# Performance work log

Measured on AMD Instinct MI355X. Metric: run time of the kernel, lower is better.

Reference implementation:

```python
import jax, jax.numpy as jnp
import numpy as np

B, S, D, H = 4, 2048, 1024, 16
DK = D // H

def setup_inputs() -> dict:
    key = jax.random.key(0)
    ks = jax.random.split(key, 5)
    std = np.sqrt(2.0 / (D + D)).astype(np.float32)
    return {
        "x": jax.random.normal(ks[0], (B, S, D), dtype=jnp.float32),
        "W_q": jax.random.normal(ks[1], (D, D), dtype=jnp.float32) * std,
        "W_k": jax.random.normal(ks[2], (D, D), dtype=jnp.float32) * std,
        "W_v": jax.random.normal(ks[3], (D, D), dtype=jnp.float32) * std,
        "W_o": jax.random.normal(ks[4], (D, D), dtype=jnp.float32) * std,
    }

def reference(x, W_q, W_k, W_v, W_o):
    b, s, d = x.shape
    # Linear layers: y = x @ W.T  (W stored as [out, in])
    q = (x @ W_q.T).reshape(b, s, H, DK).transpose(0, 2, 1, 3)  # [b,h,s,dk]
    k = (x @ W_k.T).reshape(b, s, H, DK).transpose(0, 2, 1, 3)
    v = (x @ W_v.T).reshape(b, s, H, DK).transpose(0, 2, 1, 3)
    scale = 1.0 / jnp.sqrt(jnp.asarray(DK, dtype=x.dtype))
    scores = jnp.einsum("bhqd,bhkd->bhqk", q, k) * scale  # [b,h,s,s]
    causal = jnp.tril(jnp.ones((s, s), dtype=bool))
    scores = jnp.where(causal, scores, jnp.asarray(-jnp.inf, dtype=scores.dtype))
    attn = jax.nn.softmax(scores, axis=-1)
    out = jnp.einsum("bhqk,bhkd->bhqd", attn, v)  # [b,h,s,dk]
    out = out.transpose(0, 2, 1, 3).reshape(b, s, d)
    return out @ W_o.T
```

## Files before the change

### kernel.cpp

```cpp
#include <hip/hip_runtime.h>
#include <stdint.h>

#define B_  4
#define S_  2048
#define D_  1024
#define H_  16
#define DK_ 64
#define M_  (B_ * S_)

typedef __attribute__((ext_vector_type(4))) float  f32x4;
typedef __attribute__((ext_vector_type(8))) __bf16 bf16x8;
typedef __attribute__((ext_vector_type(4))) unsigned short us4;

__device__ __forceinline__ unsigned short cvt_bf16(float f) {
  unsigned u = __float_as_uint(f);
  return (unsigned short)((u + 0x7fffu + ((u >> 16) & 1u)) >> 16);
}

__device__ __forceinline__ f32x4 mfma16(bf16x8 a, bf16x8 b, f32x4 c) {
  return __builtin_amdgcn_mfma_f32_16x16x32_bf16(a, b, c, 0, 0, 0);
}

__device__ __forceinline__ void async16(const void* g, void* l) {
  __builtin_amdgcn_global_load_lds(
      (const __attribute__((address_space(1))) void*)g,
      (__attribute__((address_space(3))) void*)l, 16, 0, 0);
}

#define XN4_ 2097152
#define WN4_ 262144
__global__ void cast_all(const float* __restrict__ x,
                         const float* __restrict__ wq,
                         const float* __restrict__ wk,
                         const float* __restrict__ wv,
                         const float* __restrict__ wo,
                         unsigned short* __restrict__ dst) {
  const int i = blockIdx.x * blockDim.x + threadIdx.x;
  const float* src;
  int k;
  if (i < XN4_) {
    src = x; k = i;
  } else {
    const int j = i - XN4_;
    const int wsel = j >> 18;
    k = j & (WN4_ - 1);
    src = (wsel == 0) ? wq : (wsel == 1) ? wk : (wsel == 2) ? wv : wo;
  }
  f32x4 v = ((const f32x4*)src)[k];
  us4 o;
  o[0] = cvt_bf16(v[0]); o[1] = cvt_bf16(v[1]);
  o[2] = cvt_bf16(v[2]); o[3] = cvt_bf16(v[3]);
  ((us4*)dst)[i] = o;
}

template <int OUTMODE>
__global__ __launch_bounds__(256) void gemm_bt(
    const unsigned short* __restrict__ A,
    const unsigned short* __restrict__ Bm,
    void* __restrict__ Cp,
    unsigned short* __restrict__ Qo, unsigned short* __restrict__ Ko,
    unsigned short* __restrict__ Vto,
    int Ndim, int Kdim) {
  constexpr int BM = 128, BN = 128, BK = 32;
  __shared__ __align__(16) unsigned short As[BM * BK];
  __shared__ __align__(16) unsigned short Bs[BN * BK];

  const int tid = threadIdx.x;
  const int w = tid >> 6, l = tid & 63;
  const int l16 = l & 15, lg = l >> 4;
  const int wr = w >> 1, wc = w & 1;
  const int rowA0 = blockIdx.y * BM;
  const int rowB0 = blockIdx.x * BN;
  const int l4 = l >> 2;
  const int lk = (l & 3) * 8;

  f32x4 acc[4][4] = {};

  for (int kt = 0; kt < Kdim; kt += BK) {
#pragma unroll
    for (int j = 0; j < 2; ++j) {
      const int chunk = j * 4 + w;
      const int r = chunk * 16 + l4;
      async16(A  + (size_t)(rowA0 + r) * Kdim + kt + lk, &As[chunk * 512]);
      async16(Bm + (size_t)(rowB0 + r) * Kdim + kt + lk, &Bs[chunk * 512]);
    }
    __syncthreads();
    bf16x8 af[4], bfr[4];
#pragma unroll
    for (int m = 0; m < 4; ++m)
      af[m] = *(const bf16x8*)&As[(wr * 64 + m * 16 + l16) * BK + lg * 8];
#pragma unroll
    for (int n = 0; n < 4; ++n)
      bfr[n] = *(const bf16x8*)&Bs[(wc * 64 + n * 16 + l16) * BK + lg * 8];
#pragma unroll
    for (int m = 0; m < 4; ++m)
#pragma unroll
      for (int n = 0; n < 4; ++n)
        acc[m][n] = mfma16(af[m], bfr[n], acc[m][n]);
    __syncthreads();
  }

  const int rb = rowA0 + wr * 64;
  const int cb = rowB0 + wc * 64;
  if constexpr (OUTMODE == 2) {
    float* C = (float*)Cp;
#pragma unroll
    for (int m = 0; m < 4; ++m)
#pragma unroll
      for (int n = 0; n < 4; ++n) {
        const int r0 = rb + m * 16 + lg * 4;
        const int c0 = cb + n * 16 + l16;
#pragma unroll
        for (int j = 0; j < 4; ++j)
          C[(size_t)(r0 + j) * Ndim + c0] = acc[m][n][j];
      }
  } else {
    const int region = cb >> 10;
    const int cbl = cb & 1023;
    if (region < 2) {
      unsigned short* C = region ? Ko : Qo;
#pragma unroll
      for (int m = 0; m < 4; ++m)
#pragma unroll
        for (int n = 0; n < 4; ++n) {
          const int r0 = rb + m * 16 + lg * 4;
          const int c0 = cbl + n * 16 + l16;
#pragma unroll
          for (int j = 0; j < 4; ++j)
            C[(size_t)(r0 + j) * 1024 + c0] = cvt_bf16(acc[m][n][j]);
        }
    } else {
#pragma unroll
      for (int m = 0; m < 4; ++m)
#pragma unroll
        for (int n = 0; n < 4; ++n) {
          const int r0 = rb + m * 16 + lg * 4;
          const int c0 = cbl + n * 16 + l16;
          us4 v;
#pragma unroll
          for (int j = 0; j < 4; ++j) v[j] = cvt_bf16(acc[m][n][j]);
          *(us4*)&Vto[((size_t)(r0 >> 11) * 1024 + c0) * 2048 + (r0 & 2047)] = v;
        }
    }
  }
}


#define KS_ 0.1803368801f

#define SMX(sc, mr, sr, oa, P, diag, rb, kv0)                                \
  do {                                                                       \
    if (diag) {                                                              \
      _Pragma("unroll") for (int nc_ = 0; nc_ < 4; ++nc_) {                  \
        const int col_ = (kv0) + nc_ * 16 + l16;                             \
        _Pragma("unroll") for (int j_ = 0; j_ < 4; ++j_)                     \
            if (col_ > (rb) + j_) sc[nc_][j_] = -INFINITY;                   \
      }                                                                      \
    }                                                                        \
    _Pragma("unroll") for (int j_ = 0; j_ < 4; ++j_) {                       \
      float t_ = fmaxf(fmaxf(sc[0][j_], sc[1][j_]),                          \
                       fmaxf(sc[2][j_], sc[3][j_]));                         \
      t_ = fmaxf(t_, __shfl_xor(t_, 1));                                     \
      t_ = fmaxf(t_, __shfl_xor(t_, 2));                                     \
      t_ = fmaxf(t_, __shfl_xor(t_, 4));                                     \
      t_ = fmaxf(t_, __shfl_xor(t_, 8));                                     \
      const bool st_ = __all(t_ <= mr[j_]);     \
      const float mnew_ = st_ ? mr[j_] : fmaxf(mr[j_], t_);                  \
      float rs_ = 0.f;                                                       \
      _Pragma("unroll") for (int nc_ = 0; nc_ < 4; ++nc_) {                  \
        const float p_ = exp2f((sc[nc_][j_] - mnew_) * KS_);                 \
        rs_ += p_;                                                           \
        P[lg * 4 + j_][nc_ * 16 + l16] = cvt_bf16(p_);                       \
      }                                                                      \
      rs_ += __shfl_xor(rs_, 1);                                             \
      rs_ += __shfl_xor(rs_, 2);                                             \
      rs_ += __shfl_xor(rs_, 4);                                             \
      rs_ += __shfl_xor(rs_, 8);                                             \
      if (st_) {                                                             \
        sr[j_] += rs_;                                                       \
      } else {                                                               \
        const float al_ = exp2f((mr[j_] - mnew_) * KS_);                     \
        sr[j_] = sr[j_] * al_ + rs_;                                         \
        mr[j_] = mnew_;                                                      \
        _Pragma("unroll") for (int d_ = 0; d_ < 4; ++d_) oa[d_][j_] *= al_;  \
      }                                                                      \
    }                                                                        \
  } while (0)

__global__ __launch_bounds__(256, 4) void flash_attn(
    const unsigned short* __restrict__ Q,
    const unsigned short* __restrict__ K,
    const unsigned short* __restrict__ Vt,
    unsigned short* __restrict__ O) {
  const int bid  = blockIdx.x;
  const int virt = (bid & 7) * 128 + (bid >> 3);
  const int bh   = virt >> 4;
  const int x    = virt & 15;
  const int b = bh >> 4, h = bh & 15;
  const int tid = threadIdx.x;
  const int w = tid >> 6, l = tid & 63;
  const int l16 = l & 15, lg = l >> 4;

  __shared__ __align__(16) unsigned short Ks[64 * 64];
  __shared__ __align__(16) unsigned short Vs[64 * 64];
  __shared__ __align__(16) unsigned short PA[4][16][72];
  __shared__ __align__(16) unsigned short PB[4][16][72];

  const int tA = x, tB = 31 - x;

  const size_t qkbase = (size_t)(b * S_) * D_ + h * DK_;
  const size_t vbase  = ((size_t)(b * D_) + h * DK_) * S_;

  const int rA = tA * 64 + w * 16 + l16;
  const int rB = tB * 64 + w * 16 + l16;
  bf16x8 qfA[2], qfB[2];
  qfA[0] = *(const bf16x8*)&Q[qkbase + (size_t)rA * D_ + lg * 8];
  qfA[1] = *(const bf16x8*)&Q[qkbase + (size_t)rA * D_ + 32 + lg * 8];
  qfB[0] = *(const bf16x8*)&Q[qkbase + (size_t)rB * D_ + lg * 8];
  qfB[1] = *(const bf16x8*)&Q[qkbase + (size_t)rB * D_ + 32 + lg * 8];

  float mA[4], sA[4], mB[4], sB[4];
  f32x4 oA[4] = {}, oB[4] = {};
#pragma unroll
  for (int j = 0; j < 4; ++j) {
    mA[j] = mB[j] = -INFINITY;
    sA[j] = sB[j] = 0.f;
  }

  const int rbA = tA * 64 + w * 16 + lg * 4;
  const int rbB = tB * 64 + w * 16 + lg * 4;

  for (int kv = 0; kv <= tB; ++kv) {
    const int kv0 = kv * 64;
    if (kv) __syncthreads();
#pragma unroll
    for (int c = 0; c < 2; ++c) {
      const int ci = c * 256 + w * 64;
      const int i  = ci + l;
      const int r  = i >> 3;
      const int cc = (i & 7) ^ (r & 7);
      async16(K  + qkbase + (size_t)(kv0 + r) * D_ + cc * 8, &Ks[ci * 8]);
      async16(Vt + vbase  + (size_t)r * S_ + kv0 + cc * 8,   &Vs[ci * 8]);
    }
    __syncthreads();

    if (kv <= tA) {
      f32x4 sc[4] = {};
      __builtin_amdgcn_s_setprio(1);
#pragma unroll
      for (int nc = 0; nc < 4; ++nc) {
        const int r = nc * 16 + l16;
#pragma unroll
        for (int ks = 0; ks < 2; ++ks) {
          const int byte = (r * 128 + ks * 64 + lg * 16) ^ ((r & 7) << 4);
          bf16x8 kf = *(const bf16x8*)((const char*)Ks + byte);
          sc[nc] = mfma16(qfA[ks], kf, sc[nc]);
        }
      }
      __builtin_amdgcn_s_setprio(0);
      SMX(sc, mA, sA, oA, PA[w], kv == tA, rbA, kv0);
      __asm__ volatile("s_waitcnt lgkmcnt(0)" ::: "memory");
      bf16x8 pa0 = *(const bf16x8*)&PA[w][l16][lg * 8];
      bf16x8 pa1 = *(const bf16x8*)&PA[w][l16][32 + lg * 8];
      __builtin_amdgcn_s_setprio(1);
#pragma unroll
      for (int d = 0; d < 4; ++d) {
        const int r = d * 16 + l16;
#pragma unroll
        for (int ks = 0; ks < 2; ++ks) {
          const int byte = (r * 128 + ks * 64 + lg * 16) ^ ((r & 7) << 4);
          bf16x8 vf = *(const bf16x8*)((const char*)Vs + byte);
          oA[d] = mfma16(ks ? pa1 : pa0, vf, oA[d]);
        }
      }
      __builtin_amdgcn_s_setprio(0);
    }

    {
      f32x4 sc[4] = {};
      __builtin_amdgcn_s_setprio(1);
#pragma unroll
      for (int nc = 0; nc < 4; ++nc) {
        const int r = nc * 16 + l16;
#pragma unroll
        for (int ks = 0; ks < 2; ++ks) {
          const int byte = (r * 128 + ks * 64 + lg * 16) ^ ((r & 7) << 4);
          bf16x8 kf = *(const bf16x8*)((const char*)Ks + byte);
          sc[nc] = mfma16(qfB[ks], kf, sc[nc]);
        }
      }
      __builtin_amdgcn_s_setprio(0);
      SMX(sc, mB, sB, oB, PB[w], kv == tB, rbB, kv0);
      __asm__ volatile("s_waitcnt lgkmcnt(0)" ::: "memory");
      bf16x8 pb0 = *(const bf16x8*)&PB[w][l16][lg * 8];
      bf16x8 pb1 = *(const bf16x8*)&PB[w][l16][32 + lg * 8];
      __builtin_amdgcn_s_setprio(1);
#pragma unroll
      for (int d = 0; d < 4; ++d) {
        const int r = d * 16 + l16;
#pragma unroll
        for (int ks = 0; ks < 2; ++ks) {
          const int byte = (r * 128 + ks * 64 + lg * 16) ^ ((r & 7) << 4);
          bf16x8 vf = *(const bf16x8*)((const char*)Vs + byte);
          oB[d] = mfma16(ks ? pb1 : pb0, vf, oB[d]);
        }
      }
      __builtin_amdgcn_s_setprio(0);
    }
  }

#pragma unroll
  for (int j = 0; j < 4; ++j) {
    const float iA = __builtin_amdgcn_rcpf(sA[j]);
    const float iB = __builtin_amdgcn_rcpf(sB[j]);
#pragma unroll
    for (int d = 0; d < 4; ++d) {
      O[((size_t)(b * S_) + rbA + j) * D_ + h * DK_ + d * 16 + l16] =
          cvt_bf16(oA[d][j] * iA);
      O[((size_t)(b * S_) + rbB + j) * D_ + h * DK_ + d * 16 + l16] =
          cvt_bf16(oB[d][j] * iB);
    }
  }
}

extern "C" void kernel_launch(void* const* d_in, const int* in_sizes, int n_in,
                              void* d_out, int out_size, void* d_ws,
                              size_t ws_size, hipStream_t stream) {
  const float* x  = (const float*)d_in[0];
  const float* Wq = (const float*)d_in[1];
  const float* Wk = (const float*)d_in[2];
  const float* Wv = (const float*)d_in[3];
  const float* Wo = (const float*)d_in[4];

  const size_t XN = (size_t)M_ * D_;
  const size_t WN = (size_t)D_ * D_;
  unsigned short* xb  = (unsigned short*)d_ws;
  unsigned short* Wqb = xb + XN;
  unsigned short* Wob = Wqb + 3 * WN;
  unsigned short* Qb  = Wob + WN;
  unsigned short* Kb  = Qb + XN;
  unsigned short* Vtb = Kb + XN;
  unsigned short* Ob  = Vtb + XN;

  cast_all<<<(XN4_ + 4 * WN4_) / 256, 256, 0, stream>>>(x, Wq, Wk, Wv, Wo, xb);

  gemm_bt<3><<<dim3(24, 64), 256, 0, stream>>>(xb, Wqb, nullptr, Qb, Kb, Vtb,
                                               3072, D_);

  flash_attn<<<dim3(1024), 256, 0, stream>>>(Qb, Kb, Vtb, Ob);

  gemm_bt<2><<<dim3(8, 64), 256, 0, stream>>>(Ob, Wob, d_out, nullptr, nullptr,
                                              nullptr, D_, D_);
}
```

Measured before the change: 318.2 us.

## Double GEMM K-tile with swizzled LDS, simplify attention softmax and drop setprio

```diff
diff --git a/kernel.cpp b/kernel.cpp
--- a/kernel.cpp
+++ b/kernel.cpp
@@ -61,7 +61,7 @@
     unsigned short* __restrict__ Qo, unsigned short* __restrict__ Ko,
     unsigned short* __restrict__ Vto,
     int Ndim, int Kdim) {
-  constexpr int BM = 128, BN = 128, BK = 32;
+  constexpr int BM = 128, BN = 128, BK = 64;
   __shared__ __align__(16) unsigned short As[BM * BK];
   __shared__ __align__(16) unsigned short Bs[BN * BK];
 
@@ -71,32 +71,41 @@
   const int wr = w >> 1, wc = w & 1;
   const int rowA0 = blockIdx.y * BM;
   const int rowB0 = blockIdx.x * BN;
-  const int l4 = l >> 2;
-  const int lk = (l & 3) * 8;
 
   f32x4 acc[4][4] = {};
 
   for (int kt = 0; kt < Kdim; kt += BK) {
 #pragma unroll
-    for (int j = 0; j < 2; ++j) {
-      const int chunk = j * 4 + w;
-      const int r = chunk * 16 + l4;
-      async16(A  + (size_t)(rowA0 + r) * Kdim + kt + lk, &As[chunk * 512]);
-      async16(Bm + (size_t)(rowB0 + r) * Kdim + kt + lk, &Bs[chunk * 512]);
+    for (int j = 0; j < 4; ++j) {
+      const int ci = j * 256 + w * 64;
+      const int i  = ci + l;
+      const int r  = i >> 3;
+      const int cc = (i & 7) ^ (r & 7);
+      async16(A  + (size_t)(rowA0 + r) * Kdim + kt + cc * 8, &As[ci * 8]);
+      async16(Bm + (size_t)(rowB0 + r) * Kdim + kt + cc * 8, &Bs[ci * 8]);
     }
     __syncthreads();
-    bf16x8 af[4], bfr[4];
-#pragma unroll
-    for (int m = 0; m < 4; ++m)
-      af[m] = *(const bf16x8*)&As[(wr * 64 + m * 16 + l16) * BK + lg * 8];
-#pragma unroll
-    for (int n = 0; n < 4; ++n)
-      bfr[n] = *(const bf16x8*)&Bs[(wc * 64 + n * 16 + l16) * BK + lg * 8];
-#pragma unroll
-    for (int m = 0; m < 4; ++m)
-#pragma unroll
-      for (int n = 0; n < 4; ++n)
-        acc[m][n] = mfma16(af[m], bfr[n], acc[m][n]);
+#pragma unroll
+    for (int hf = 0; hf < 2; ++hf) {
+      bf16x8 af[4], bfr[4];
+#pragma unroll
+      for (int m = 0; m < 4; ++m) {
+        const int r = wr * 64 + m * 16 + l16;
+        const int byte = (r * 128) + ((lg * 16 + hf * 64) ^ ((r & 7) << 4));
+        af[m] = *(const bf16x8*)((const char*)As + byte);
+      }
+#pragma unroll
+      for (int n = 0; n < 4; ++n) {
+        const int r = wc * 64 + n * 16 + l16;
+        const int byte = (r * 128) + ((lg * 16 + hf * 64) ^ ((r & 7) << 4));
+        bfr[n] = *(const bf16x8*)((const char*)Bs + byte);
+      }
+#pragma unroll
+      for (int m = 0; m < 4; ++m)
+#pragma unroll
+        for (int n = 0; n < 4; ++n)
+          acc[m][n] = mfma16(af[m], bfr[n], acc[m][n]);
+    }
     __syncthreads();
   }
 
@@ -146,10 +155,11 @@
 }
 
 
-#define KS_ 0.1803368801f
-
 #define SMX(sc, mr, sr, oa, P, diag, rb, kv0)                                \
   do {                                                                       \
+    _Pragma("unroll") for (int nc_ = 0; nc_ < 4; ++nc_)                      \
+        _Pragma("unroll") for (int j_ = 0; j_ < 4; ++j_)                     \
+            sc[nc_][j_] *= 0.125f;                                           \
     if (diag) {                                                              \
       _Pragma("unroll") for (int nc_ = 0; nc_ < 4; ++nc_) {                  \
         const int col_ = (kv0) + nc_ * 16 + l16;                             \
@@ -164,11 +174,10 @@
       t_ = fmaxf(t_, __shfl_xor(t_, 2));                                     \
       t_ = fmaxf(t_, __shfl_xor(t_, 4));                                     \
       t_ = fmaxf(t_, __shfl_xor(t_, 8));                                     \
-      const bool st_ = __all(t_ <= mr[j_]);     \
-      const float mnew_ = st_ ? mr[j_] : fmaxf(mr[j_], t_);                  \
+      const float mnew_ = fmaxf(mr[j_], t_);                                 \
       float rs_ = 0.f;                                                       \
       _Pragma("unroll") for (int nc_ = 0; nc_ < 4; ++nc_) {                  \
-        const float p_ = exp2f((sc[nc_][j_] - mnew_) * KS_);                 \
+        const float p_ = __expf(sc[nc_][j_] - mnew_);                        \
         rs_ += p_;                                                           \
         P[lg * 4 + j_][nc_ * 16 + l16] = cvt_bf16(p_);                       \
       }                                                                      \
@@ -176,14 +185,10 @@
       rs_ += __shfl_xor(rs_, 2);                                             \
       rs_ += __shfl_xor(rs_, 4);                                             \
       rs_ += __shfl_xor(rs_, 8);                                             \
-      if (st_) {                                                             \
-        sr[j_] += rs_;                                                       \
-      } else {                                                               \
-        const float al_ = exp2f((mr[j_] - mnew_) * KS_);                     \
-        sr[j_] = sr[j_] * al_ + rs_;                                         \
-        mr[j_] = mnew_;                                                      \
-        _Pragma("unroll") for (int d_ = 0; d_ < 4; ++d_) oa[d_][j_] *= al_;  \
-      }                                                                      \
+      const float al_ = __expf(mr[j_] - mnew_);                              \
+      sr[j_] = sr[j_] * al_ + rs_;                                           \
+      mr[j_] = mnew_;                                                        \
+      _Pragma("unroll") for (int d_ = 0; d_ < 4; ++d_) oa[d_][j_] *= al_;    \
     }                                                                        \
   } while (0)
 
@@ -246,7 +251,6 @@
 
     if (kv <= tA) {
       f32x4 sc[4] = {};
-      __builtin_amdgcn_s_setprio(1);
 #pragma unroll
       for (int nc = 0; nc < 4; ++nc) {
         const int r = nc * 16 + l16;
@@ -257,12 +261,10 @@
           sc[nc] = mfma16(qfA[ks], kf, sc[nc]);
         }
       }
-      __builtin_amdgcn_s_setprio(0);
       SMX(sc, mA, sA, oA, PA[w], kv == tA, rbA, kv0);
       __asm__ volatile("s_waitcnt lgkmcnt(0)" ::: "memory");
       bf16x8 pa0 = *(const bf16x8*)&PA[w][l16][lg * 8];
       bf16x8 pa1 = *(const bf16x8*)&PA[w][l16][32 + lg * 8];
-      __builtin_amdgcn_s_setprio(1);
 #pragma unroll
       for (int d = 0; d < 4; ++d) {
         const int r = d * 16 + l16;
@@ -273,12 +275,10 @@
           oA[d] = mfma16(ks ? pa1 : pa0, vf, oA[d]);
         }
       }
-      __builtin_amdgcn_s_setprio(0);
     }
 
     {
       f32x4 sc[4] = {};
-      __builtin_amdgcn_s_setprio(1);
 #pragma unroll
       for (int nc = 0; nc < 4; ++nc) {
         const int r = nc * 16 + l16;
@@ -289,12 +289,10 @@
           sc[nc] = mfma16(qfB[ks], kf, sc[nc]);
         }
       }
-      __builtin_amdgcn_s_setprio(0);
       SMX(sc, mB, sB, oB, PB[w], kv == tB, rbB, kv0);
       __asm__ volatile("s_waitcnt lgkmcnt(0)" ::: "memory");
       bf16x8 pb0 = *(const bf16x8*)&PB[w][l16][lg * 8];
       bf16x8 pb1 = *(const bf16x8*)&PB[w][l16][32 + lg * 8];
-      __builtin_amdgcn_s_setprio(1);
 #pragma unroll
       for (int d = 0; d < 4; ++d) {
         const int r = d * 16 + l16;
@@ -305,22 +303,18 @@
           oB[d] = mfma16(ks ? pb1 : pb0, vf, oB[d]);
         }
       }
-      __builtin_amdgcn_s_setprio(0);
-    }
-  }
-
-#pragma unroll
-  for (int j = 0; j < 4; ++j) {
-    const float iA = __builtin_amdgcn_rcpf(sA[j]);
-    const float iB = __builtin_amdgcn_rcpf(sB[j]);
-#pragma unroll
-    for (int d = 0; d < 4; ++d) {
+    }
+  }
+
+#pragma unroll
+  for (int d = 0; d < 4; ++d)
+#pragma unroll
+    for (int j = 0; j < 4; ++j) {
       O[((size_t)(b * S_) + rbA + j) * D_ + h * DK_ + d * 16 + l16] =
-          cvt_bf16(oA[d][j] * iA);
+          cvt_bf16(oA[d][j] / sA[j]);
       O[((size_t)(b * S_) + rbB + j) * D_ + h * DK_ + d * 16 + l16] =
-          cvt_bf16(oB[d][j] * iB);
-    }
-  }
+          cvt_bf16(oB[d][j] / sB[j]);
+    }
 }
 
 extern "C" void kernel_launch(void* const* d_in, const int* in_sizes, int n_in,
```

New measurement: 304.9 us. 4.2% less time.
